# Kernel tuning notes

Hardware: AMD Instinct MI355X
Metric: run time of the kernel (lower is better)

Reference implementation:

```python
import jax, jax.numpy as jnp
import numpy as np

DIM, HEADS, DHEAD = 256, 8, 64
HID = HEADS * DHEAD


def _elu1(x):
    # F.elu(x) + 1 == exp(x) for x<0, x+1 for x>=0
    return jnp.where(x > 0, x + 1.0, jnp.exp(x))


def setup_inputs() -> dict:
    key = jax.random.key(0)
    ks = jax.random.split(key, 6)
    B, H, W = 8, 64, 64
    x = jax.random.normal(ks[0], (B, DIM, H, W), dtype=jnp.float32)
    contact_map = jax.random.uniform(ks[1], (B, 1, H, W), dtype=jnp.float32)
    s_qkv = 1.0 / np.sqrt(DIM)
    Wqkv = jax.random.normal(ks[2], (3 * HID, DIM), dtype=jnp.float32) * s_qkv
    s_out = 1.0 / np.sqrt(HID)
    Wout = jax.random.normal(ks[3], (DIM, HID), dtype=jnp.float32) * s_out
    bout = jax.random.normal(ks[4], (DIM,), dtype=jnp.float32) * 0.01
    contact_scale = jnp.float32(0.1)
    return {"x": x, "contact_map": contact_map, "Wqkv": Wqkv,
            "Wout": Wout, "bout": bout, "contact_scale": contact_scale}


def reference(x, contact_map, Wqkv, Wout, bout, contact_scale):
    b, c, h, w = x.shape
    n = h * w
    xf = x.reshape(b, c, n)                                  # b c n
    qkv = jnp.einsum('oc,bcn->bon', Wqkv, xf)                # b (3*H*D) n
    qkv = qkv.reshape(b, 3, HEADS, DHEAD, n)                 # qkv-major channel order
    q = _elu1(qkv[:, 0])                                     # b h d n
    k = _elu1(qkv[:, 1])
    v = qkv[:, 2]
    cm = contact_map.reshape(b, 1, 1, n)                     # b 1 1 n
    k = k * (1.0 + contact_scale * cm)
    kv = jnp.einsum('bhdn,bhen->bhde', k, v)                 # b h d e
    ksum = k.sum(axis=-1)                                    # b h d
    z = 1.0 / (jnp.einsum('bhdn,bhd->bhn', q, ksum) + 1e-6)  # b h n
    out = jnp.einsum('bhde,bhdn->bhne', kv, q) * z[..., None]  # b h n e
    out = out.transpose(0, 1, 3, 2).reshape(b, HID, n)       # b (h d) n
    y = jnp.einsum('oc,bcn->bon', Wout, out) + bout[None, :, None]
    return y.reshape(b, -1, h, w)
```

## Files before the change

kernel.cpp:

```cpp
#include <hip/hip_runtime.h>
#include <stdint.h>


#define NPIX 4096
#define HIDC 512
#define DIMC 256
#define BATCH 8

typedef __attribute__((ext_vector_type(8))) short bf16x8;
typedef __attribute__((ext_vector_type(4))) float f32x4;
typedef __attribute__((ext_vector_type(16))) float f32x16;

__device__ __forceinline__ float bf2f(unsigned short h) {
    unsigned int u = ((unsigned int)h) << 16; float f;
    __builtin_memcpy(&f, &u, 4); return f;
}
__device__ __forceinline__ unsigned short f2bf(float f) {
    unsigned int u; __builtin_memcpy(&u, &f, 4);
    u += 0x7fffu + ((u >> 16) & 1u);
    return (unsigned short)(u >> 16);
}
__device__ __forceinline__ float elu1(float x) {
    return x > 0.f ? x + 1.f : __expf(x);
}
__device__ __forceinline__ void gl16(const unsigned short* g, unsigned short* l) {
    __builtin_amdgcn_global_load_lds(
        (__attribute__((address_space(1))) const void*)g,
        (__attribute__((address_space(3))) void*)l, 16, 0, 0);
}

__global__ __launch_bounds__(256) void k_convW(
    const float* __restrict__ Wqkv, const float* __restrict__ Wout,
    unsigned short* __restrict__ Wb, unsigned short* __restrict__ Wob)
{
    int i4 = (blockIdx.x * 256 + threadIdx.x) * 4;
    const int NW1 = 1536 * 256;
    float4 v; unsigned short* dst;
    if (i4 < NW1) { v = *(const float4*)&Wqkv[i4]; dst = Wb + i4; }
    else { int j = i4 - NW1; v = *(const float4*)&Wout[j]; dst = Wob + j; }
    ushort4 o; o.x = f2bf(v.x); o.y = f2bf(v.y); o.z = f2bf(v.z); o.w = f2bf(v.w);
    *(ushort4*)dst = o;
}

__global__ __launch_bounds__(256) void k_tx(
    const float* __restrict__ x, unsigned short* __restrict__ xT)
{
    __shared__ float tile[32][33];
    const int n0 = blockIdx.x * 32, c0 = blockIdx.y * 32, b = blockIdx.z;
    const int t = threadIdx.x;
    const int r = t >> 3, c4 = (t & 7) * 4;
    float4 v = *(const float4*)&x[((size_t)b * DIMC + c0 + r) * NPIX + n0 + c4];
    tile[r][c4 + 0] = v.x; tile[r][c4 + 1] = v.y;
    tile[r][c4 + 2] = v.z; tile[r][c4 + 3] = v.w;
    __syncthreads();
    ushort4 o;
    unsigned short* op = (unsigned short*)&o;
#pragma unroll
    for (int i = 0; i < 4; i++) op[i] = f2bf(tile[c4 + i][r]);
    *(ushort4*)&xT[((size_t)b * NPIX + n0 + r) * DIMC + c0 + c4] = o;
}

__global__ __launch_bounds__(256) void k_fused(
    const unsigned short* __restrict__ xT,
    const unsigned short* __restrict__ Wb,
    const float* __restrict__ cmp,
    const float* __restrict__ csp,
    unsigned short* __restrict__ qT,
    float* __restrict__ kvp,
    float* __restrict__ ksump)
{
    const int b  = blockIdx.z;
    const int m0 = blockIdx.x * 128;
    const int yb = blockIdx.y;
    const int h  = yb - 4;
    const int t = threadIdx.x;
    const int wave = t >> 6, lane = t & 63;
    const int wm = wave >> 1, wn = wave & 1;
    const int l31 = lane & 31, lhi = lane >> 5;

    __shared__ unsigned short sh[128 * 128];
    unsigned short* As  = sh;
    unsigned short* Bs  = sh + 128 * 64;
    unsigned short* kvS = sh;

    const unsigned short* Ag = xT + ((size_t)b * NPIX + m0) * DIMC;

    f32x16 acc[2][2];
#pragma unroll
    for (int i = 0; i < 2; i++)
#pragma unroll
        for (int j = 0; j < 2; j++)
#pragma unroll
            for (int r = 0; r < 16; r++) acc[i][j][r] = 0.f;

    const int r8  = lane >> 3;
    const int jg8 = (((lane & 7) ^ r8) & 7) * 8;
    const int xsw = (l31 & 7);

    for (int k0 = 0; k0 < DIMC; k0 += 64) {
#pragma unroll
        for (int i = 0; i < 4; i++) {
            const int rowg = wave * 32 + i * 8;
            const int arow = rowg + r8;
            gl16(&Ag[(size_t)arow * DIMC + k0 + jg8], &As[rowg * 64]);
            int wrow;
            if (yb < 4) wrow = yb * 128 + arow;
            else wrow = (arow < 64) ? (512 + h * 64 + arow)
                                    : (1024 + h * 64 + (arow - 64));
            gl16(&Wb[(size_t)wrow * DIMC + k0 + jg8], &Bs[rowg * 64]);
        }
        __syncthreads();
#pragma unroll
        for (int ks = 0; ks < 4; ks++) {
            const int coff = ((ks * 2 + lhi) ^ xsw) * 8;
            bf16x8 af[2], bfg[2];
#pragma unroll
            for (int fm = 0; fm < 2; fm++)
                af[fm] = *(const bf16x8*)&As[(wm * 64 + fm * 32 + l31) * 64 + coff];
#pragma unroll
            for (int fn = 0; fn < 2; fn++)
                bfg[fn] = *(const bf16x8*)&Bs[(wn * 64 + fn * 32 + l31) * 64 + coff];
#pragma unroll
            for (int fm = 0; fm < 2; fm++)
#pragma unroll
                for (int fn = 0; fn < 2; fn++)
                    acc[fm][fn] = __builtin_amdgcn_mfma_f32_32x32x16_bf16(
                        af[fm], bfg[fn], acc[fm][fn], 0, 0, 0);
        }
        __syncthreads();
    }

    if (yb < 4) {
        const int n0 = yb * 128;
#pragma unroll
        for (int fm = 0; fm < 2; fm++) {
            const int pbase = m0 + wm * 64 + fm * 32;
#pragma unroll
            for (int fn = 0; fn < 2; fn++) {
                const int o = n0 + wn * 64 + fn * 32 + l31;
#pragma unroll
                for (int r = 0; r < 16; r++) {
                    int prow = pbase + (r & 3) + 8 * (r >> 2) + 4 * lhi;
                    qT[((size_t)b * NPIX + prow) * HIDC + o] = f2bf(elu1(acc[fm][fn][r]));
                }
            }
        }
        return;
    }

    const float cs = *csp;
    float gv4[2];
#pragma unroll
    for (int fm = 0; fm < 2; fm++)
        gv4[fm] = 1.f + cs * cmp[(size_t)b * NPIX + m0 + wm * 64 + fm * 32 + l31];

    float ks0 = 0.f, ks1 = 0.f;
#pragma unroll
    for (int fm = 0; fm < 2; fm++) {
#pragma unroll
        for (int r = 0; r < 16; r++) {
            const int rp = (r & 3) + 8 * (r >> 2) + 4 * lhi;
            const float g = __shfl(gv4[fm], rp);
            const int px = wm * 64 + fm * 32 + rp;
#pragma unroll
            for (int fn = 0; fn < 2; fn++) {
                const int o = wn * 64 + fn * 32 + l31;
                float val = acc[fm][fn][r];
                unsigned short st;
                if (o < 64) {
                    float kvl = elu1(val) * g;
                    if (fn == 0) ks0 += kvl; else ks1 += kvl;
                    st = f2bf(kvl);
                } else {
                    st = f2bf(val);
                }
                kvS[(size_t)o * 128 + (px ^ ((o & 7) << 3))] = st;
            }
        }
    }
    if (wn == 0) {
        atomicAdd(&ksump[(size_t)(b * 8 + h) * 64 + l31], ks0);
        atomicAdd(&ksump[(size_t)(b * 8 + h) * 64 + 32 + l31], ks1);
    }
    __syncthreads();

    f32x16 kva;
#pragma unroll
    for (int r = 0; r < 16; r++) kva[r] = 0.f;
#pragma unroll
    for (int pk = 0; pk < 8; pk++) {
        const int co = ((pk * 2 + lhi) ^ (l31 & 7)) * 8;
        bf16x8 kf = *(const bf16x8*)&kvS[(size_t)(wm * 32 + l31) * 128 + co];
        bf16x8 vf = *(const bf16x8*)&kvS[(size_t)(64 + wn * 32 + l31) * 128 + co];
        kva = __builtin_amdgcn_mfma_f32_32x32x16_bf16(kf, vf, kva, 0, 0, 0);
    }
    float* kvb = kvp + (size_t)(b * 8 + h) * 4096;
#pragma unroll
    for (int r = 0; r < 16; r++) {
        const int d = wm * 32 + (r & 3) + 8 * (r >> 2) + 4 * lhi;
        atomicAdd(&kvb[(size_t)d * 64 + wn * 32 + l31], kva[r]);
    }
}

#define LS3 72
__global__ __launch_bounds__(256) void k_out(
    const unsigned short* __restrict__ qT,
    const float* __restrict__ kv, const float* __restrict__ ksum,
    unsigned short* __restrict__ outT)
{
    const int bh = blockIdx.y, p0 = blockIdx.x * 128;
    const int b = bh >> 3, h = bh & 7;
    const int t = threadIdx.x, wave = t >> 6, lane = t & 63;
    const int l31 = lane & 31, lhi = lane >> 5;

    __shared__ unsigned short Aq[128 * LS3];
    __shared__ unsigned short Bv[96 * LS3];

    const unsigned short* qg = qT + ((size_t)b * NPIX + p0) * HIDC + h * 64;
#pragma unroll
    for (int i = 0; i < 4; i++) {
        int idx = t + i * 256;
        int row = idx >> 3, c8 = (idx & 7) * 8;
        *(uint4*)&Aq[row * LS3 + c8] = *(const uint4*)&qg[(size_t)row * HIDC + c8];
    }
    const float* kvg = kv + (size_t)bh * 4096;
#pragma unroll
    for (int i = 0; i < 16; i++) {
        int idx = t + i * 256;
        int d = idx >> 6, e = idx & 63;
        Bv[e * LS3 + d] = f2bf(kvg[idx]);
    }
    if (t < 64) {
        float ksv = ksum[bh * 64 + t];
        unsigned short hi = f2bf(ksv);
        Bv[64 * LS3 + t] = hi;
        Bv[65 * LS3 + t] = f2bf(ksv - bf2f(hi));
    }
    for (int i = t; i < 30 * 64; i += 256)
        Bv[(66 + (i >> 6)) * LS3 + (i & 63)] = 0;
    __syncthreads();

    f32x16 acc[3];
#pragma unroll
    for (int j = 0; j < 3; j++)
#pragma unroll
        for (int r = 0; r < 16; r++) acc[j][r] = 0.f;

#pragma unroll
    for (int ksub = 0; ksub < 4; ksub++) {
        const int koff = ksub * 16 + lhi * 8;
        bf16x8 af = *(const bf16x8*)&Aq[(wave * 32 + l31) * LS3 + koff];
#pragma unroll
        for (int nf = 0; nf < 3; nf++) {
            bf16x8 bfg = *(const bf16x8*)&Bv[(nf * 32 + l31) * LS3 + koff];
            acc[nf] = __builtin_amdgcn_mfma_f32_32x32x16_bf16(af, bfg, acc[nf], 0, 0, 0);
        }
    }

    unsigned short* og = outT + ((size_t)b * NPIX + p0 + wave * 32) * HIDC + h * 64;
#pragma unroll
    for (int r = 0; r < 16; r++) {
        float hi = __shfl(acc[2][r], lane & 32);
        float lo = __shfl(acc[2][r], (lane & 32) | 1);
        float z = 1.f / (hi + lo + 1e-6f);
        int prow = (r & 3) + 8 * (r >> 2) + 4 * lhi;
#pragma unroll
        for (int nf = 0; nf < 2; nf++)
            og[(size_t)prow * HIDC + nf * 32 + l31] = f2bf(acc[nf][r] * z);
    }
}

__global__ __launch_bounds__(256) void k_y(
    const unsigned short* __restrict__ outT,
    const unsigned short* __restrict__ Wob,
    const float* __restrict__ bout,
    float* __restrict__ y)
{
    const int b  = blockIdx.z;
    const int m0 = blockIdx.x * 128;
    const int n0 = blockIdx.y * 128;
    const int t = threadIdx.x;
    const int wave = t >> 6, lane = t & 63;
    const int wm = wave >> 1, wn = wave & 1;
    const int lrow = lane & 15, quad = lane >> 4;

    __shared__ unsigned short As[128 * 64];
    __shared__ unsigned short Bs[128 * 64];

    const unsigned short* Ag = outT + ((size_t)b * NPIX + m0) * HIDC;
    const unsigned short* Bg = Wob + (size_t)n0 * HIDC;

    f32x4 acc[4][4];
#pragma unroll
    for (int i = 0; i < 4; i++)
#pragma unroll
        for (int j = 0; j < 4; j++) acc[i][j] = (f32x4){0.f, 0.f, 0.f, 0.f};

    const int r8  = lane >> 3;
    const int jg8 = (((lane & 7) ^ r8) & 7) * 8;
    const int xswA = (lrow & 7);

    for (int k0 = 0; k0 < HIDC; k0 += 64) {
#pragma unroll
        for (int i = 0; i < 4; i++) {
            const int rowg = wave * 32 + i * 8;
            gl16(&Ag[(size_t)(rowg + r8) * HIDC + k0 + jg8], &As[rowg * 64]);
            gl16(&Bg[(size_t)(rowg + r8) * HIDC + k0 + jg8], &Bs[rowg * 64]);
        }
        __syncthreads();
#pragma unroll
        for (int ksb = 0; ksb < 2; ksb++) {
            bf16x8 af[4], bfr[4];
#pragma unroll
            for (int mt = 0; mt < 4; mt++) {
                const int row = wm * 64 + mt * 16 + lrow;
                af[mt] = *(const bf16x8*)&As[row * 64 + (((ksb * 4 + quad) ^ xswA)) * 8];
            }
#pragma unroll
            for (int nt = 0; nt < 4; nt++) {
                const int row = wn * 64 + nt * 16 + lrow;
                bfr[nt] = *(const bf16x8*)&Bs[row * 64 + (((ksb * 4 + quad) ^ xswA)) * 8];
            }
#pragma unroll
            for (int mt = 0; mt < 4; mt++)
#pragma unroll
                for (int nt = 0; nt < 4; nt++)
                    acc[mt][nt] = __builtin_amdgcn_mfma_f32_16x16x32_bf16(
                        af[mt], bfr[nt], acc[mt][nt], 0, 0, 0);
        }
        __syncthreads();
    }

#pragma unroll
    for (int mt = 0; mt < 4; mt++) {
        const int pixel0 = m0 + wm * 64 + mt * 16 + quad * 4;
#pragma unroll
        for (int nt = 0; nt < 4; nt++) {
            const int o = n0 + wn * 64 + nt * 16 + lrow;
            const float bias = bout[o];
            f32x4 a = acc[mt][nt];
            float4 st; st.x = a[0] + bias; st.y = a[1] + bias;
            st.z = a[2] + bias; st.w = a[3] + bias;
            *(float4*)&y[((size_t)b * DIMC + o) * NPIX + pixel0] = st;
        }
    }
}

extern "C" void kernel_launch(void* const* d_in, const int* in_sizes, int n_in,
                              void* d_out, int out_size, void* d_ws, size_t ws_size,
                              hipStream_t stream) {
    (void)in_sizes; (void)n_in; (void)out_size; (void)ws_size;
    const float* x    = (const float*)d_in[0];
    const float* cm   = (const float*)d_in[1];
    const float* Wqkv = (const float*)d_in[2];
    const float* Wout = (const float*)d_in[3];
    const float* bout = (const float*)d_in[4];
    const float* csp  = (const float*)d_in[5];
    float* y = (float*)d_out;

    const size_t qn = (size_t)BATCH * HIDC * NPIX;
    char* ws = (char*)d_ws;
    unsigned short* qT   = (unsigned short*)ws;                 ws += qn * 2;
    unsigned short* outT = (unsigned short*)ws;                 ws += qn * 2;
    unsigned short* xT   = outT;
    float* kvp   = (float*)ws;                                  ws += (size_t)64 * 64 * 64 * 4;
    float* ksump = (float*)ws;                                  ws += (size_t)64 * 64 * 4;
    unsigned short* Wb  = (unsigned short*)ws;                  ws += (size_t)1536 * 256 * 2;
    unsigned short* Wob = (unsigned short*)ws;

    hipMemsetAsync(kvp, 0, ((size_t)64 * 64 * 64 + 64 * 64) * sizeof(float), stream);
    k_convW<<<512, 256, 0, stream>>>(Wqkv, Wout, Wb, Wob);
    k_tx   <<<dim3(128, 8, 8), 256, 0, stream>>>(x, xT);
    k_fused<<<dim3(32, 12, 8), 256, 0, stream>>>(xT, Wb, cm, csp, qT, kvp, ksump);
    k_out  <<<dim3(32, 64),    256, 0, stream>>>(qT, kvp, ksump, outT);
    k_y    <<<dim3(32, 2, 8),  256, 0, stream>>>(outT, Wob, bout, y);
}
```

Before: 218.2 us.

## Replace kv atomicAdd reduction with per-block partials and separate reduce kernel

Each k_fused block now writes its 64x64 kv partial to a dedicated slot instead of atomically adding into a shared buffer, and a new k_kvred kernel sums the 32 partials per batch-head. This removes contended float atomics, at the cost of an extra launch and about 32 MB of partial writes and reads. The k/v staging into shared memory is also packed into 4-element vector stores, with the contact-map shuffles hoisted out of the loop.

```diff
diff --git a/kernel.cpp b/kernel.cpp
--- a/kernel.cpp
+++ b/kernel.cpp
@@ -66,7 +66,7 @@
     const float* __restrict__ cmp,
     const float* __restrict__ csp,
     unsigned short* __restrict__ qT,
-    float* __restrict__ kvp,
+    float* __restrict__ kvq,
     float* __restrict__ ksump)
 {
     const int b  = blockIdx.z;
@@ -149,36 +149,48 @@
     }
 
     const float cs = *csp;
+    const bool isK = (wn == 0);
     float gv4[2];
 #pragma unroll
     for (int fm = 0; fm < 2; fm++)
         gv4[fm] = 1.f + cs * cmp[(size_t)b * NPIX + m0 + wm * 64 + fm * 32 + l31];
 
+    float gk[2][16];
+#pragma unroll
+    for (int fm = 0; fm < 2; fm++)
+#pragma unroll
+        for (int r = 0; r < 16; r++)
+            gk[fm][r] = __shfl(gv4[fm], (r & 3) + 8 * (r >> 2) + 4 * lhi);
+
     float ks0 = 0.f, ks1 = 0.f;
 #pragma unroll
     for (int fm = 0; fm < 2; fm++) {
 #pragma unroll
-        for (int r = 0; r < 16; r++) {
-            const int rp = (r & 3) + 8 * (r >> 2) + 4 * lhi;
-            const float g = __shfl(gv4[fm], rp);
-            const int px = wm * 64 + fm * 32 + rp;
-#pragma unroll
-            for (int fn = 0; fn < 2; fn++) {
-                const int o = wn * 64 + fn * 32 + l31;
-                float val = acc[fm][fn][r];
-                unsigned short st;
-                if (o < 64) {
-                    float kvl = elu1(val) * g;
-                    if (fn == 0) ks0 += kvl; else ks1 += kvl;
-                    st = f2bf(kvl);
-                } else {
-                    st = f2bf(val);
+        for (int fn = 0; fn < 2; fn++) {
+            const int o = wn * 64 + fn * 32 + l31;
+            const int sw = (o & 7) << 3;
+#pragma unroll
+            for (int rg = 0; rg < 4; rg++) {
+                ushort4 pk4;
+                unsigned short* pp = (unsigned short*)&pk4;
+#pragma unroll
+                for (int j = 0; j < 4; j++) {
+                    const int r = rg * 4 + j;
+                    float val = acc[fm][fn][r];
+                    if (isK) {
+                        float kvl = elu1(val) * gk[fm][r];
+                        if (fn == 0) ks0 += kvl; else ks1 += kvl;
+                        pp[j] = f2bf(kvl);
+                    } else {
+                        pp[j] = f2bf(val);
+                    }
                 }
-                kvS[(size_t)o * 128 + (px ^ ((o & 7) << 3))] = st;
+                const int px0 = wm * 64 + fm * 32 + rg * 8 + 4 * lhi;
+                *(ushort4*)&kvS[(size_t)o * 128 + (px0 ^ sw)] = pk4;
             }
         }
     }
-    if (wn == 0) {
+    if (isK) {
         atomicAdd(&ksump[(size_t)(b * 8 + h) * 64 + l31], ks0);
         atomicAdd(&ksump[(size_t)(b * 8 + h) * 64 + 32 + l31], ks1);
     }
@@ -194,12 +206,27 @@
         bf16x8 vf = *(const bf16x8*)&kvS[(size_t)(64 + wn * 32 + l31) * 128 + co];
         kva = __builtin_amdgcn_mfma_f32_32x32x16_bf16(kf, vf, kva, 0, 0, 0);
     }
-    float* kvb = kvp + (size_t)(b * 8 + h) * 4096;
+    float* kvb = kvq + ((size_t)(b * 8 + h) * 32 + blockIdx.x) * 4096;
 #pragma unroll
     for (int r = 0; r < 16; r++) {
         const int d = wm * 32 + (r & 3) + 8 * (r >> 2) + 4 * lhi;
-        atomicAdd(&kvb[(size_t)d * 64 + wn * 32 + l31], kva[r]);
-    }
+        kvb[(size_t)d * 64 + wn * 32 + l31] = kva[r];
+    }
+}
+
+__global__ __launch_bounds__(256) void k_kvred(
+    const float* __restrict__ kvq, float* __restrict__ kvp)
+{
+    const int bh = blockIdx.x >> 2, q4 = blockIdx.x & 3;
+    const float4* src = (const float4*)(kvq + (size_t)bh * 32 * 4096)
+                      + q4 * 256 + threadIdx.x;
+    float4 s; s.x = 0.f; s.y = 0.f; s.z = 0.f; s.w = 0.f;
+#pragma unroll 8
+    for (int i = 0; i < 32; i++) {
+        float4 v = src[(size_t)i * 1024];
+        s.x += v.x; s.y += v.y; s.z += v.z; s.w += v.w;
+    }
+    ((float4*)(kvp + (size_t)bh * 4096))[q4 * 256 + threadIdx.x] = s;
 }
 
 #define LS3 72
@@ -365,13 +392,15 @@
     unsigned short* xT   = outT;
     float* kvp   = (float*)ws;                                  ws += (size_t)64 * 64 * 64 * 4;
     float* ksump = (float*)ws;                                  ws += (size_t)64 * 64 * 4;
+    float* kvq   = (float*)ws;                                  ws += (size_t)64 * 32 * 4096 * 4;
     unsigned short* Wb  = (unsigned short*)ws;                  ws += (size_t)1536 * 256 * 2;
     unsigned short* Wob = (unsigned short*)ws;
 
-    hipMemsetAsync(kvp, 0, ((size_t)64 * 64 * 64 + 64 * 64) * sizeof(float), stream);
+    hipMemsetAsync(ksump, 0, (size_t)64 * 64 * sizeof(float), stream);
     k_convW<<<512, 256, 0, stream>>>(Wqkv, Wout, Wb, Wob);
     k_tx   <<<dim3(128, 8, 8), 256, 0, stream>>>(x, xT);
-    k_fused<<<dim3(32, 12, 8), 256, 0, stream>>>(xT, Wb, cm, csp, qT, kvp, ksump);
+    k_fused<<<dim3(32, 12, 8), 256, 0, stream>>>(xT, Wb, cm, csp, qT, kvq, ksump);
+    k_kvred<<<256, 256, 0, stream>>>(kvq, kvp);
     k_out  <<<dim3(32, 64),    256, 0, stream>>>(qT, kvp, ksump, outT);
     k_y    <<<dim3(32, 2, 8),  256, 0, stream>>>(outT, Wob, bout, y);
 }
```

After: 210.1 us. 3.7% less time.
